# Performance work log

Hardware: AMD Instinct MI355X
Metric: run time of the kernel (lower is better)

The kernel has to match this reference:

```python
import jax, jax.numpy as jnp
import numpy as np
from jax.scipy.special import logsumexp

C = 1024   # num HMM states
H = 256    # hidden_dim
V = 10000  # vocab size
B = 16     # batch
N = 256    # sequence length
EPS = 1e-5


def _layernorm(x, g, b):
    mu = x.mean(-1, keepdims=True)
    var = ((x - mu) ** 2).mean(-1, keepdims=True)
    return g * (x - mu) * jax.lax.rsqrt(var + EPS) + b


def _residual(x, W1, b1, W2, b2, g, beta):
    # ResidualLayer: ln(relu(lin2(relu(lin1(x)))) + relu(lin1(x))), dropout=0
    h = jax.nn.relu(x @ W1.T + b1)
    return _layernorm(jax.nn.relu(h @ W2.T + b2) + h, g, beta)


def setup_inputs() -> dict:
    key = jax.random.key(0)
    ks = iter(jax.random.split(key, 40))
    def nrm(shape, scale):
        return jax.random.normal(next(ks), shape, dtype=jnp.float32) * scale
    w = 1.0 / np.sqrt(H)
    inp = {}
    # embeddings (torch.randn)
    inp['start_emb'] = nrm((C, H), 1.0)
    inp['state_emb'] = nrm((C, H), 1.0)
    inp['pre_emb'] = nrm((C, H), 1.0)
    # start_mlp: ResidualLayer(H,H) + Linear(H,1)
    for p, out_dim in (('s', 1), ('t', C), ('e', V)):
        inp[p + '_W1'] = nrm((H, H), w)
        inp[p + '_b1'] = jnp.zeros((H,), jnp.float32)
        inp[p + '_W2'] = nrm((H, H), w)
        inp[p + '_b2'] = jnp.zeros((H,), jnp.float32)
        inp[p + '_g'] = jnp.ones((H,), jnp.float32)
        inp[p + '_beta'] = jnp.zeros((H,), jnp.float32)
        inp[p + '_Wo'] = nrm((out_dim, H), w)
        inp[p + '_bo'] = jnp.zeros((out_dim,), jnp.float32)
    inp['text'] = jax.random.randint(next(ks), (B, N), 0, V)
    return inp


def reference(start_emb, state_emb, pre_emb,
              s_W1, s_b1, s_W2, s_b2, s_g, s_beta, s_Wo, s_bo,
              t_W1, t_b1, t_W2, t_b2, t_g, t_beta, t_Wo, t_bo,
              e_W1, e_b1, e_W2, e_b2, e_g, e_beta, e_Wo, e_bo,
              text):
    # start: (C,) log init distribution
    start = jax.nn.log_softmax(
        (_residual(start_emb, s_W1, s_b1, s_W2, s_b2, s_g, s_beta) @ s_Wo.T + s_bo).squeeze(-1))
    # transition[i, j] = log p(z_t = j | z_{t-1} = i), shape (C, C)
    transition = jax.nn.log_softmax(
        _residual(state_emb, t_W1, t_b1, t_W2, t_b2, t_g, t_beta) @ t_Wo.T + t_bo, axis=-1)
    # emission[c, v] = log p(x = v | z = c), shape (C, V)
    emission = jax.nn.log_softmax(
        _residual(pre_emb, e_W1, e_b1, e_W2, e_b2, e_g, e_beta) @ e_Wo.T + e_bo, axis=-1)

    emit = emission.T[text]              # (B, N, C): log p(x_t | z_t = c)
    alpha0 = start[None, :] + emit[:, 0]  # (B, C)

    def step(alpha, e_t):
        # log-semiring matmul: alpha_next[b,j] = lse_i(alpha[b,i] + T[i,j]) + emit
        a = logsumexp(alpha[:, :, None] + transition[None], axis=1) + e_t
        return a, None

    alphaT, _ = jax.lax.scan(step, alpha0, jnp.swapaxes(emit[:, 1:], 0, 1))
    return logsumexp(alphaT, axis=-1).sum()
```

## Files before the change

kernel.cpp:

```cpp
#include <hip/hip_runtime.h>
#include <hip/hip_bf16.h>

typedef __attribute__((ext_vector_type(8))) short short8;
typedef __attribute__((ext_vector_type(4))) float f32x4;
typedef unsigned short ushort;
typedef unsigned long long u64;
typedef unsigned int u32;

#define AL(p) __hip_atomic_load((p), __ATOMIC_RELAXED, __HIP_MEMORY_SCOPE_AGENT)
#define AS(p,v) __hip_atomic_store((p), (v), __ATOMIC_RELAXED, __HIP_MEMORY_SCOPE_AGENT)

__device__ inline ushort f2bf(float x) {
  __hip_bfloat16 h = __float2bfloat16(x);
  return *reinterpret_cast<ushort*>(&h);
}
__device__ inline float bfhi2f(u32 lo) {
  union { u32 u; float f; } c; c.u = lo & 0xFFFF0000u; return c.f;
}
__device__ inline float bflo2f(u32 lo) {
  union { u32 u; float f; } c; c.u = lo << 16; return c.f;
}
__device__ inline u32 pk2(float a, float b) {
  return (u32)f2bf(__expf(a)) | ((u32)f2bf(__expf(b)) << 16);
}

__global__ __launch_bounds__(256) void mlp3_kernel(
    const float* X0, const float* W10, const float* b10, const float* W20, const float* b20,
    const float* g0, const float* be0, float* of0, ushort* ob0,
    const float* X1, const float* W11, const float* b11, const float* W21, const float* b21,
    const float* g1, const float* be1, float* of1, ushort* ob1,
    const float* X2, const float* W12, const float* b12, const float* W22, const float* b22,
    const float* g2, const float* be2, float* of2, ushort* ob2,
    const float* ca_i, ushort* ca_o, int nc_a,
    const float* cb_i, ushort* cb_o, int nc_b)
{
  int y = blockIdx.y;
  if (y == 3) {
    int i = blockIdx.x * 256 + threadIdx.x;
    int st = 64 * 256;
    for (; i < nc_a + nc_b; i += st) {
      if (i < nc_a) ca_o[i] = f2bf(ca_i[i]);
      else          cb_o[i - nc_a] = f2bf(cb_i[i - nc_a]);
    }
    return;
  }
  const float *X, *W1, *b1, *W2, *b2, *g, *beta; float* of32; ushort* obf;
  if (y == 0)      { X=X0; W1=W10; b1=b10; W2=W20; b2=b20; g=g0; beta=be0; of32=of0; obf=ob0; }
  else if (y == 1) { X=X1; W1=W11; b1=b11; W2=W21; b2=b21; g=g1; beta=be1; of32=of1; obf=ob1; }
  else             { X=X2; W1=W12; b1=b12; W2=W22; b2=b22; g=g2; beta=be2; of32=of2; obf=ob2; }

  __shared__ float Xs[16 * 260];
  __shared__ float H1s[16 * 260];
  __shared__ float mu_s[16], rs_s[16];
  int tid = threadIdx.x;
  int r0 = blockIdx.x * 16;
  for (int q = 0; q < 16; ++q) Xs[q * 260 + tid] = X[(r0 + q) * 256 + tid];
  __syncthreads();
  int r = tid & 15, jg = tid >> 4;
  for (int jj = 0; jj < 16; ++jj) {
    int j = jg * 16 + jj;
    const float4* wrow = (const float4*)(W1 + j * 256);
    const float4* xrow = (const float4*)(Xs + r * 260);
    float acc = 0.f;
#pragma unroll 8
    for (int kq = 0; kq < 64; ++kq) {
      float4 w = wrow[kq], x = xrow[kq];
      acc += w.x * x.x + w.y * x.y + w.z * x.z + w.w * x.w;
    }
    acc += b1[j];
    H1s[r * 260 + j] = acc > 0.f ? acc : 0.f;
  }
  __syncthreads();
  for (int jj = 0; jj < 16; ++jj) {
    int j = jg * 16 + jj;
    const float4* wrow = (const float4*)(W2 + j * 256);
    const float4* hrow = (const float4*)(H1s + r * 260);
    float acc = 0.f;
#pragma unroll 8
    for (int kq = 0; kq < 64; ++kq) {
      float4 w = wrow[kq], x = hrow[kq];
      acc += w.x * x.x + w.y * x.y + w.z * x.z + w.w * x.w;
    }
    acc += b2[j];
    float v = (acc > 0.f ? acc : 0.f) + H1s[r * 260 + j];
    Xs[r * 260 + j] = v;
  }
  __syncthreads();
  if (tid < 16) {
    float s = 0.f, s2 = 0.f;
    for (int k = 0; k < 256; ++k) { float x = Xs[tid * 260 + k]; s += x; s2 += x * x; }
    float mu = s * (1.0f / 256.0f);
    float var = s2 * (1.0f / 256.0f) - mu * mu;
    mu_s[tid] = mu; rs_s[tid] = rsqrtf(var + 1e-5f);
  }
  __syncthreads();
  for (int q = 0; q < 16; ++q) {
    float x = (Xs[q * 260 + tid] - mu_s[q]) * rs_s[q] * g[tid] + beta[tid];
    if (of32) of32[(r0 + q) * 256 + tid] = x;
    if (obf)  obf[(r0 + q) * 256 + tid] = f2bf(x);
  }
}

__global__ __launch_bounds__(1024) void shead_kernel(
    const float* __restrict__ h, const float* __restrict__ Wo, const float* __restrict__ bo,
    float* __restrict__ start)
{
  __shared__ float red[16];
  __shared__ float lse_s;
  int tid = threadIdx.x;
  const float4* wr = (const float4*)Wo;
  const float4* hr = (const float4*)(h + tid * 256);
  float acc = 0.f;
  for (int kq = 0; kq < 64; ++kq) {
    float4 w = wr[kq], x = hr[kq];
    acc += w.x * x.x + w.y * x.y + w.z * x.z + w.w * x.w;
  }
  acc += bo[0];
  float s = __expf(acc);
  for (int m = 1; m < 64; m <<= 1) s += __shfl_xor(s, m);
  if ((tid & 63) == 0) red[tid >> 6] = s;
  __syncthreads();
  if (tid == 0) {
    float t = 0.f;
    for (int w = 0; w < 16; ++w) t += red[w];
    lse_s = logf(t);
  }
  __syncthreads();
  start[tid] = acc - lse_s;
}

__global__ __launch_bounds__(256) void gemm_kernel(
    const ushort* __restrict__ A, const ushort* __restrict__ Bw,
    int mode, int Nvalid, int chunks,
    const float* __restrict__ bias,
    float* __restrict__ out, float* __restrict__ esum, const int* __restrict__ text)
{
  __shared__ ushort As[64 * 264];
  __shared__ ushort Bs[32 * 264];
  int tid = threadIdx.x;
  int m0 = blockIdx.x * 64;
#pragma unroll
  for (int q = 0; q < 8; ++q) {
    int idx = q * 256 + tid;
    int row = idx >> 5, c8 = idx & 31;
    *(short8*)(As + row * 264 + c8 * 8) = *(const short8*)(A + (m0 + row) * 256 + c8 * 8);
  }
  int lane = tid & 63, wave = tid >> 6;
  int r16 = lane & 15, quad = lane >> 4;
  float sacc[4] = {0.f, 0.f, 0.f, 0.f};

  for (int c = 0; c < chunks; ++c) {
    int n0 = (blockIdx.y * chunks + c) * 32;
    if (c) __syncthreads();
#pragma unroll
    for (int q = 0; q < 4; ++q) {
      int idx = q * 256 + tid;
      int row = idx >> 5, c8 = idx & 31;
      int grow = n0 + row;
      short8 val = {0, 0, 0, 0, 0, 0, 0, 0};
      if (mode == 2) {
        int v = text[(grow & 15) * 256 + (grow >> 4)];
        val = *(const short8*)(Bw + v * 256 + c8 * 8);
      } else if (grow < Nvalid) {
        val = *(const short8*)(Bw + grow * 256 + c8 * 8);
      }
      *(short8*)(Bs + row * 264 + c8 * 8) = val;
    }
    __syncthreads();
    f32x4 acc0 = {0.f, 0.f, 0.f, 0.f}, acc1 = {0.f, 0.f, 0.f, 0.f};
#pragma unroll
    for (int kb = 0; kb < 8; ++kb) {
      short8 a  = *(const short8*)(As + (wave * 16 + r16) * 264 + kb * 32 + quad * 8);
      short8 b0 = *(const short8*)(Bs + r16 * 264 + kb * 32 + quad * 8);
      short8 b1 = *(const short8*)(Bs + (16 + r16) * 264 + kb * 32 + quad * 8);
      acc0 = __builtin_amdgcn_mfma_f32_16x16x32_bf16(a, b0, acc0, 0, 0, 0);
      acc1 = __builtin_amdgcn_mfma_f32_16x16x32_bf16(a, b1, acc1, 0, 0, 0);
    }
    if (mode == 0) {
#pragma unroll
      for (int rr = 0; rr < 4; ++rr) {
        int row = m0 + wave * 16 + quad * 4 + rr;
        int c0 = n0 + r16, c1 = n0 + 16 + r16;
        out[row * 1024 + c0] = acc0[rr] + bias[c0];
        out[row * 1024 + c1] = acc1[rr] + bias[c1];
      }
    } else if (mode == 1) {
#pragma unroll
      for (int rr = 0; rr < 4; ++rr) {
        int c0 = n0 + r16, c1 = n0 + 16 + r16;
        float p0 = (c0 < Nvalid) ? __expf(acc0[rr] + bias[c0]) : 0.f;
        float p1 = (c1 < Nvalid) ? __expf(acc1[rr] + bias[c1]) : 0.f;
        sacc[rr] += p0 + p1;
      }
    } else {
      int c0 = m0 + wave * 16 + quad * 4;
      int tb0 = n0 + r16, tb1 = n0 + 16 + r16;
      int v0 = text[(tb0 & 15) * 256 + (tb0 >> 4)];
      int v1 = text[(tb1 & 15) * 256 + (tb1 >> 4)];
      float l0 = logf(esum[c0]), l1 = logf(esum[c0 + 1]);
      float l2 = logf(esum[c0 + 2]), l3 = logf(esum[c0 + 3]);
      float4 o0, o1;
      o0.x = acc0[0] + bias[v0] - l0; o0.y = acc0[1] + bias[v0] - l1;
      o0.z = acc0[2] + bias[v0] - l2; o0.w = acc0[3] + bias[v0] - l3;
      o1.x = acc1[0] + bias[v1] - l0; o1.y = acc1[1] + bias[v1] - l1;
      o1.z = acc1[2] + bias[v1] - l2; o1.w = acc1[3] + bias[v1] - l3;
      *(float4*)(out + tb0 * 1024 + c0) = o0;
      *(float4*)(out + tb1 * 1024 + c0) = o1;
    }
  }
  if (mode == 1) {
#pragma unroll
    for (int rr = 0; rr < 4; ++rr) {
      float s = sacc[rr];
      s += __shfl_xor(s, 1); s += __shfl_xor(s, 2);
      s += __shfl_xor(s, 4); s += __shfl_xor(s, 8);
      if (r16 == 0) atomicAdd(esum + m0 + wave * 16 + quad * 4 + rr, s);
    }
  }
}

__global__ __launch_bounds__(256) void trans_kernel(
    const float* __restrict__ logits, ushort* __restrict__ texp_frag)
{
  __shared__ float red[4];
  __shared__ float lse_s;
  int i = blockIdx.x, tid = threadIdx.x;
  float x[4];
  float s = 0.f;
#pragma unroll
  for (int q = 0; q < 4; ++q) { x[q] = logits[i * 1024 + q * 256 + tid]; s += __expf(x[q]); }
  for (int m = 1; m < 64; m <<= 1) s += __shfl_xor(s, m);
  if ((tid & 63) == 0) red[tid >> 6] = s;
  __syncthreads();
  if (tid == 0) lse_s = logf(red[0] + red[1] + red[2] + red[3]);
  __syncthreads();
  float lse = lse_s;
  int kblk = i >> 5, quad = (i >> 3) & 3, idx = i & 7;
#pragma unroll
  for (int q = 0; q < 4; ++q) {
    int j = q * 256 + tid;
    int pos = (((j >> 4) * 32 + kblk) * 64 + quad * 16 + (j & 15)) * 8 + idx;
    texp_frag[pos] = f2bf(__expf(x[q] - lse));
  }
}

__global__ __launch_bounds__(256, 1) void scan_kernel(
    const ushort* __restrict__ texp_frag,
    const float* __restrict__ emitg,
    const float* __restrict__ start_v,
    u64* __restrict__ abuf,
    float* __restrict__ out)
{
  __shared__ __align__(16) char Asb[2][4 * 2080];
  __shared__ float redw[4][4], reds[4][4];

  int tid = threadIdx.x, lane = tid & 63, wave = tid >> 6;
  int r16 = lane & 15, quad = lane >> 4;
  int p = blockIdx.x, bg = p & 3, cb = p >> 2;
  int b0 = bg * 4;

  const short8* tg = (const short8*)texp_frag + (size_t)cb * 8192 + wave * 2048;
  short8 treg[32];
#pragma unroll
  for (int k = 0; k < 32; ++k) treg[k] = tg[k * 64 + lane];
#pragma unroll
  for (int k = 0; k < 32; ++k) asm volatile("" : "+a"(treg[k]));

  int colw = cb * 64 + wave * 16 + r16;
  int abase = (r16 & 3) * 2080 + quad * 16;

  float m_r[4], Bs[4];
#pragma unroll
  for (int i = 0; i < 4; ++i) {
    m_r[i] = start_v[0] + emitg[(size_t)(b0 + i) * 1024];
    Bs[i] = m_r[i];
  }
  {
    int c0 = 2 * tid, c2 = 2 * tid + 512;
    char* ab = Asb[1];
#pragma unroll
    for (int r = 0; r < 4; ++r) {
      const float* eb = emitg + (size_t)(b0 + r) * 1024;
      float v0 = start_v[c0] + eb[c0],     v1 = start_v[c0 + 1] + eb[c0 + 1];
      float v2 = start_v[c2] + eb[c2],     v3 = start_v[c2 + 1] + eb[c2 + 1];
      *(u32*)(ab + r * 2080 + 4 * tid)        = pk2(v0 - m_r[r], v1 - m_r[r]);
      *(u32*)(ab + r * 2080 + 1024 + 4 * tid) = pk2(v2 - m_r[r], v3 - m_r[r]);
    }
  }
  __syncthreads();

  for (int t = 1; t < 256; ++t) {
    float e0 = 0.f, e1 = 0.f, e2 = 0.f, e3 = 0.f;
    if (quad == 0) {
      const float* ep = emitg + (size_t)(t * 16 + b0) * 1024 + colw;
      e0 = ep[0]; e1 = ep[1024]; e2 = ep[2048]; e3 = ep[3072];
    }

    const char* ab = Asb[t & 1];
    f32x4 a0, a1, a2, a3;
    {
      short8 f0 = *(const short8*)(ab + abase);
      short8 f1 = *(const short8*)(ab + abase + 64);
      short8 f2 = *(const short8*)(ab + abase + 128);
      short8 f3 = *(const short8*)(ab + abase + 192);
      asm volatile("v_mfma_f32_16x16x32_bf16 %0, %1, %2, 0" : "=v"(a0) : "v"(f0), "a"(treg[0]));
      asm volatile("v_mfma_f32_16x16x32_bf16 %0, %1, %2, 0" : "=v"(a1) : "v"(f1), "a"(treg[1]));
      asm volatile("v_mfma_f32_16x16x32_bf16 %0, %1, %2, 0" : "=v"(a2) : "v"(f2), "a"(treg[2]));
      asm volatile("v_mfma_f32_16x16x32_bf16 %0, %1, %2, 0" : "=v"(a3) : "v"(f3), "a"(treg[3]));
    }
#pragma unroll
    for (int kb = 4; kb < 32; kb += 4) {
      short8 f0 = *(const short8*)(ab + abase + kb * 64);
      short8 f1 = *(const short8*)(ab + abase + kb * 64 + 64);
      short8 f2 = *(const short8*)(ab + abase + kb * 64 + 128);
      short8 f3 = *(const short8*)(ab + abase + kb * 64 + 192);
      asm volatile("v_mfma_f32_16x16x32_bf16 %0, %1, %2, %0" : "+v"(a0) : "v"(f0), "a"(treg[kb + 0]));
      asm volatile("v_mfma_f32_16x16x32_bf16 %0, %1, %2, %0" : "+v"(a1) : "v"(f1), "a"(treg[kb + 1]));
      asm volatile("v_mfma_f32_16x16x32_bf16 %0, %1, %2, %0" : "+v"(a2) : "v"(f2), "a"(treg[kb + 2]));
      asm volatile("v_mfma_f32_16x16x32_bf16 %0, %1, %2, %0" : "+v"(a3) : "v"(f3), "a"(treg[kb + 3]));
    }
    asm volatile("s_nop 7\n\ts_nop 7\n\ts_nop 1"
                 : "+v"(a0), "+v"(a1), "+v"(a2), "+v"(a3));
    f32x4 acc = (a0 + a1) + (a2 + a3);

    if (quad == 0) {
      float d0 = __logf(acc[0]) + e0;
      float d1 = __logf(acc[1]) + e1;
      float d2 = __logf(acc[2]) + e2;
      float d3 = __logf(acc[3]) + e3;
      u64 tag = ((u64)(u32)t) << 32;
      u64* ob = abuf + (t & 1) * 8192 + bg * 2048 + colw;
      AS(ob,        tag | (u64)((u32)f2bf(d0) | ((u32)f2bf(d1) << 16)));
      AS(ob + 1024, tag | (u64)((u32)f2bf(d2) | ((u32)f2bf(d3) << 16)));
    }

    if (t < 255) {
      u64 x0, x1, x2, x3, x4, x5, x6, x7, n0, n1;
      {
        const u64* buf = abuf + (t & 1) * 8192 + bg * 2048;
        int oa = 2 * tid, oc = 2 * tid + 512;
        u32 want = (u32)t;
        bool first = true;
        for (;;) {
          if (!first) __builtin_amdgcn_s_sleep(1);
          first = false;
          x0 = AL(buf + oa);        x1 = AL(buf + oa + 1);
          x2 = AL(buf + oc);        x3 = AL(buf + oc + 1);
          x4 = AL(buf + 1024 + oa); x5 = AL(buf + 1024 + oa + 1);
          x6 = AL(buf + 1024 + oc); x7 = AL(buf + 1024 + oc + 1);
          n0 = AL(buf);             n1 = AL(buf + 1024);
          u32 bad = ((u32)(x0 >> 32) ^ want) | ((u32)(x1 >> 32) ^ want) |
                    ((u32)(x2 >> 32) ^ want) | ((u32)(x3 >> 32) ^ want) |
                    ((u32)(x4 >> 32) ^ want) | ((u32)(x5 >> 32) ^ want) |
                    ((u32)(x6 >> 32) ^ want) | ((u32)(x7 >> 32) ^ want) |
                    ((u32)(n0 >> 32) ^ want) | ((u32)(n1 >> 32) ^ want);
          if (bad == 0) break;
        }
      }
      m_r[0] = bflo2f((u32)n0); m_r[1] = bfhi2f((u32)n0);
      m_r[2] = bflo2f((u32)n1); m_r[3] = bfhi2f((u32)n1);
      Bs[0] += m_r[0]; Bs[1] += m_r[1]; Bs[2] += m_r[2]; Bs[3] += m_r[3];

      char* aw = Asb[(t + 1) & 1];
      u32 l0 = (u32)x0, l1 = (u32)x1, l2 = (u32)x2, l3 = (u32)x3;
      u32 l4 = (u32)x4, l5 = (u32)x5, l6 = (u32)x6, l7 = (u32)x7;
      *(u32*)(aw + 4 * tid)                = pk2(bflo2f(l0) - m_r[0], bflo2f(l1) - m_r[0]);
      *(u32*)(aw + 1024 + 4 * tid)         = pk2(bflo2f(l2) - m_r[0], bflo2f(l3) - m_r[0]);
      *(u32*)(aw + 2080 + 4 * tid)         = pk2(bfhi2f(l0) - m_r[1], bfhi2f(l1) - m_r[1]);
      *(u32*)(aw + 2080 + 1024 + 4 * tid)  = pk2(bfhi2f(l2) - m_r[1], bfhi2f(l3) - m_r[1]);
      *(u32*)(aw + 4160 + 4 * tid)         = pk2(bflo2f(l4) - m_r[2], bflo2f(l5) - m_r[2]);
      *(u32*)(aw + 4160 + 1024 + 4 * tid)  = pk2(bflo2f(l6) - m_r[2], bflo2f(l7) - m_r[2]);
      *(u32*)(aw + 6240 + 4 * tid)         = pk2(bfhi2f(l4) - m_r[3], bfhi2f(l5) - m_r[3]);
      *(u32*)(aw + 6240 + 1024 + 4 * tid)  = pk2(bfhi2f(l6) - m_r[3], bfhi2f(l7) - m_r[3]);
      __syncthreads();
    }
  }

  if (cb == 0) {
    const u64* fb = abuf + 8192 + bg * 2048;
    int oa = 2 * tid, oc = 2 * tid + 512;
    u64 x0, x1, x2, x3, x4, x5, x6, x7;
    {
      bool first = true;
      for (;;) {
        if (!first) __builtin_amdgcn_s_sleep(1);
        first = false;
        x0 = AL(fb + oa);        x1 = AL(fb + oa + 1);
        x2 = AL(fb + oc);        x3 = AL(fb + oc + 1);
        x4 = AL(fb + 1024 + oa); x5 = AL(fb + 1024 + oa + 1);
        x6 = AL(fb + 1024 + oc); x7 = AL(fb + 1024 + oc + 1);
        u32 bad = ((u32)(x0 >> 32) ^ 255u) | ((u32)(x1 >> 32) ^ 255u) |
                  ((u32)(x2 >> 32) ^ 255u) | ((u32)(x3 >> 32) ^ 255u) |
                  ((u32)(x4 >> 32) ^ 255u) | ((u32)(x5 >> 32) ^ 255u) |
                  ((u32)(x6 >> 32) ^ 255u) | ((u32)(x7 >> 32) ^ 255u);
        if (bad == 0) break;
      }
    }
    float bv[4][4];
    bv[0][0] = bflo2f((u32)x0); bv[0][1] = bflo2f((u32)x1); bv[0][2] = bflo2f((u32)x2); bv[0][3] = bflo2f((u32)x3);
    bv[1][0] = bfhi2f((u32)x0); bv[1][1] = bfhi2f((u32)x1); bv[1][2] = bfhi2f((u32)x2); bv[1][3] = bfhi2f((u32)x3);
    bv[2][0] = bflo2f((u32)x4); bv[2][1] = bflo2f((u32)x5); bv[2][2] = bflo2f((u32)x6); bv[2][3] = bflo2f((u32)x7);
    bv[3][0] = bfhi2f((u32)x4); bv[3][1] = bfhi2f((u32)x5); bv[3][2] = bfhi2f((u32)x6); bv[3][3] = bfhi2f((u32)x7);
    float M[4], S[4];
#pragma unroll
    for (int i = 0; i < 4; ++i)
      M[i] = fmaxf(fmaxf(bv[i][0], bv[i][1]), fmaxf(bv[i][2], bv[i][3]));
    for (int off = 1; off < 64; off <<= 1) {
#pragma unroll
      for (int i = 0; i < 4; ++i) M[i] = fmaxf(M[i], __shfl_xor(M[i], off));
    }
    if (lane == 0) { redw[wave][0]=M[0]; redw[wave][1]=M[1]; redw[wave][2]=M[2]; redw[wave][3]=M[3]; }
    __syncthreads();
#pragma unroll
    for (int i = 0; i < 4; ++i)
      M[i] = fmaxf(fmaxf(redw[0][i], redw[1][i]), fmaxf(redw[2][i], redw[3][i]));
#pragma unroll
    for (int i = 0; i < 4; ++i)
      S[i] = __expf(bv[i][0] - M[i]) + __expf(bv[i][1] - M[i]) +
             __expf(bv[i][2] - M[i]) + __expf(bv[i][3] - M[i]);
    for (int off = 1; off < 64; off <<= 1) {
#pragma unroll
      for (int i = 0; i < 4; ++i) S[i] += __shfl_xor(S[i], off);
    }
    if (lane == 0) { reds[wave][0]=S[0]; reds[wave][1]=S[1]; reds[wave][2]=S[2]; reds[wave][3]=S[3]; }
    __syncthreads();
    if (tid == 0) {
      float tot = 0.f;
#pragma unroll
      for (int i = 0; i < 4; ++i) {
        float Sg = reds[0][i] + reds[1][i] + reds[2][i] + reds[3][i];
        tot += Bs[i] + M[i] + logf(Sg);
      }
      atomicAdd(out, tot);
    }
  }
}

extern "C" void kernel_launch(void* const* d_in, const int* in_sizes, int n_in,
                              void* d_out, int out_size, void* d_ws, size_t ws_size,
                              hipStream_t stream)
{
  (void)in_sizes; (void)n_in; (void)out_size; (void)ws_size;
  const float* start_emb = (const float*)d_in[0];
  const float* state_emb = (const float*)d_in[1];
  const float* pre_emb   = (const float*)d_in[2];
  const float* s_W1 = (const float*)d_in[3];  const float* s_b1 = (const float*)d_in[4];
  const float* s_W2 = (const float*)d_in[5];  const float* s_b2 = (const float*)d_in[6];
  const float* s_g  = (const float*)d_in[7];  const float* s_be = (const float*)d_in[8];
  const float* s_Wo = (const float*)d_in[9];  const float* s_bo = (const float*)d_in[10];
  const float* t_W1 = (const float*)d_in[11]; const float* t_b1 = (const float*)d_in[12];
  const float* t_W2 = (const float*)d_in[13]; const float* t_b2 = (const float*)d_in[14];
  const float* t_g  = (const float*)d_in[15]; const float* t_be = (const float*)d_in[16];
  const float* t_Wo = (const float*)d_in[17]; const float* t_bo = (const float*)d_in[18];
  const float* e_W1 = (const float*)d_in[19]; const float* e_b1 = (const float*)d_in[20];
  const float* e_W2 = (const float*)d_in[21]; const float* e_b2 = (const float*)d_in[22];
  const float* e_g  = (const float*)d_in[23]; const float* e_be = (const float*)d_in[24];
  const float* e_Wo = (const float*)d_in[25]; const float* e_bo = (const float*)d_in[26];
  const int*   text = (const int*)d_in[27];
  float* out = (float*)d_out;

  char* ws = (char*)d_ws;
  size_t off = 0;
  auto alloc = [&](size_t bytes) -> char* {
    char* p = ws + off;
    off = (off + bytes + 255) & ~(size_t)255;
    return p;
  };
  float* esum       = (float*)alloc(1024 * 4);
  u64*   abuf       = (u64*)alloc(2 * 8192 * 8);
  float* start_v    = (float*)alloc(1024 * 4);
  float* h_s        = (float*)alloc(1024 * 256 * 4);
  ushort* h_t_bf    = (ushort*)alloc(1024 * 256 * 2);
  ushort* h_e_bf    = (ushort*)alloc(1024 * 256 * 2);
  ushort* tWo_bf    = (ushort*)alloc(1024 * 256 * 2);
  ushort* eWo_bf    = (ushort*)alloc(10000 * 256 * 2);
  float* tlogits    = (float*)alloc(1024 * 1024 * 4);
  ushort* texp_frag = (ushort*)alloc(1024 * 1024 * 2);
  float* emitg      = (float*)alloc(4096 * 1024 * 4);

  hipMemsetAsync(ws, 0, 4096 + 2 * 8192 * 8, stream);
  hipMemsetAsync(d_out, 0, 4, stream);

  mlp3_kernel<<<dim3(64, 4), 256, 0, stream>>>(
      start_emb, s_W1, s_b1, s_W2, s_b2, s_g, s_be, h_s, nullptr,
      state_emb, t_W1, t_b1, t_W2, t_b2, t_g, t_be, nullptr, h_t_bf,
      pre_emb,  e_W1, e_b1, e_W2, e_b2, e_g, e_be, nullptr, h_e_bf,
      t_Wo, tWo_bf, 1024 * 256, e_Wo, eWo_bf, 10000 * 256);

  shead_kernel<<<1, 1024, 0, stream>>>(h_s, s_Wo, s_bo, start_v);

  gemm_kernel<<<dim3(16, 32),  256, 0, stream>>>(h_t_bf, tWo_bf, 0, 1024,  1, t_bo, tlogits, nullptr, nullptr);
  trans_kernel<<<1024, 256, 0, stream>>>(tlogits, texp_frag);
  gemm_kernel<<<dim3(16, 40),  256, 0, stream>>>(h_e_bf, eWo_bf, 1, 10000, 8, e_bo, nullptr, esum, nullptr);
  gemm_kernel<<<dim3(16, 128), 256, 0, stream>>>(h_e_bf, eWo_bf, 2, 4096,  1, e_bo, emitg, esum, text);

  scan_kernel<<<64, 256, 0, stream>>>(texp_frag, emitg, start_v, abuf, out);
}
```

Before: 913.8 us.

## Halve scan blocks; each wave computes two 16-column transition tiles

```diff
diff --git a/kernel.cpp b/kernel.cpp
--- a/kernel.cpp
+++ b/kernel.cpp
@@ -259,14 +259,18 @@
   int p = blockIdx.x, bg = p & 3, cb = p >> 2;
   int b0 = bg * 4;
 
-  const short8* tg = (const short8*)texp_frag + (size_t)cb * 8192 + wave * 2048;
-  short8 treg[32];
-#pragma unroll
-  for (int k = 0; k < 32; ++k) treg[k] = tg[k * 64 + lane];
-#pragma unroll
-  for (int k = 0; k < 32; ++k) asm volatile("" : "+a"(treg[k]));
-
-  int colw = cb * 64 + wave * 16 + r16;
+  const short8* tg = (const short8*)texp_frag + (size_t)(cb * 8 + wave * 2) * 2048;
+  short8 tA[32], tB[32];
+#pragma unroll
+  for (int k = 0; k < 32; ++k) tA[k] = tg[k * 64 + lane];
+#pragma unroll
+  for (int k = 0; k < 32; ++k) tB[k] = tg[2048 + k * 64 + lane];
+#pragma unroll
+  for (int k = 0; k < 32; ++k) asm volatile("" : "+a"(tA[k]));
+#pragma unroll
+  for (int k = 0; k < 32; ++k) asm volatile("" : "+a"(tB[k]));
+
+  int colw = cb * 128 + wave * 32 + r16;
   int abase = (r16 & 3) * 2080 + quad * 16;
 
   float m_r[4], Bs[4];
@@ -291,22 +295,28 @@
 
   for (int t = 1; t < 256; ++t) {
     float e0 = 0.f, e1 = 0.f, e2 = 0.f, e3 = 0.f;
+    float e4 = 0.f, e5 = 0.f, e6 = 0.f, e7 = 0.f;
     if (quad == 0) {
       const float* ep = emitg + (size_t)(t * 16 + b0) * 1024 + colw;
-      e0 = ep[0]; e1 = ep[1024]; e2 = ep[2048]; e3 = ep[3072];
+      e0 = ep[0];  e1 = ep[1024]; e2 = ep[2048]; e3 = ep[3072];
+      e4 = ep[16]; e5 = ep[1040]; e6 = ep[2064]; e7 = ep[3088];
     }
 
     const char* ab = Asb[t & 1];
-    f32x4 a0, a1, a2, a3;
+    f32x4 a0, a1, a2, a3, c0, c1, c2, c3;
     {
       short8 f0 = *(const short8*)(ab + abase);
       short8 f1 = *(const short8*)(ab + abase + 64);
       short8 f2 = *(const short8*)(ab + abase + 128);
       short8 f3 = *(const short8*)(ab + abase + 192);
-      asm volatile("v_mfma_f32_16x16x32_bf16 %0, %1, %2, 0" : "=v"(a0) : "v"(f0), "a"(treg[0]));
-      asm volatile("v_mfma_f32_16x16x32_bf16 %0, %1, %2, 0" : "=v"(a1) : "v"(f1), "a"(treg[1]));
-      asm volatile("v_mfma_f32_16x16x32_bf16 %0, %1, %2, 0" : "=v"(a2) : "v"(f2), "a"(treg[2]));
-      asm volatile("v_mfma_f32_16x16x32_bf16 %0, %1, %2, 0" : "=v"(a3) : "v"(f3), "a"(treg[3]));
+      asm volatile("v_mfma_f32_16x16x32_bf16 %0, %1, %2, 0" : "=v"(a0) : "v"(f0), "a"(tA[0]));
+      asm volatile("v_mfma_f32_16x16x32_bf16 %0, %1, %2, 0" : "=v"(a1) : "v"(f1), "a"(tA[1]));
+      asm volatile("v_mfma_f32_16x16x32_bf16 %0, %1, %2, 0" : "=v"(a2) : "v"(f2), "a"(tA[2]));
+      asm volatile("v_mfma_f32_16x16x32_bf16 %0, %1, %2, 0" : "=v"(a3) : "v"(f3), "a"(tA[3]));
+      asm volatile("v_mfma_f32_16x16x32_bf16 %0, %1, %2, 0" : "=v"(c0) : "v"(f0), "a"(tB[0]));
+      asm volatile("v_mfma_f32_16x16x32_bf16 %0, %1, %2, 0" : "=v"(c1) : "v"(f1), "a"(tB[1]));
+      asm volatile("v_mfma_f32_16x16x32_bf16 %0, %1, %2, 0" : "=v"(c2) : "v"(f2), "a"(tB[2]));
+      asm volatile("v_mfma_f32_16x16x32_bf16 %0, %1, %2, 0" : "=v"(c3) : "v"(f3), "a"(tB[3]));
     }
 #pragma unroll
     for (int kb = 4; kb < 32; kb += 4) {
@@ -314,24 +324,36 @@
       short8 f1 = *(const short8*)(ab + abase + kb * 64 + 64);
       short8 f2 = *(const short8*)(ab + abase + kb * 64 + 128);
       short8 f3 = *(const short8*)(ab + abase + kb * 64 + 192);
-      asm volatile("v_mfma_f32_16x16x32_bf16 %0, %1, %2, %0" : "+v"(a0) : "v"(f0), "a"(treg[kb + 0]));
-      asm volatile("v_mfma_f32_16x16x32_bf16 %0, %1, %2, %0" : "+v"(a1) : "v"(f1), "a"(treg[kb + 1]));
-      asm volatile("v_mfma_f32_16x16x32_bf16 %0, %1, %2, %0" : "+v"(a2) : "v"(f2), "a"(treg[kb + 2]));
-      asm volatile("v_mfma_f32_16x16x32_bf16 %0, %1, %2, %0" : "+v"(a3) : "v"(f3), "a"(treg[kb + 3]));
+      asm volatile("v_mfma_f32_16x16x32_bf16 %0, %1, %2, %0" : "+v"(a0) : "v"(f0), "a"(tA[kb + 0]));
+      asm volatile("v_mfma_f32_16x16x32_bf16 %0, %1, %2, %0" : "+v"(a1) : "v"(f1), "a"(tA[kb + 1]));
+      asm volatile("v_mfma_f32_16x16x32_bf16 %0, %1, %2, %0" : "+v"(a2) : "v"(f2), "a"(tA[kb + 2]));
+      asm volatile("v_mfma_f32_16x16x32_bf16 %0, %1, %2, %0" : "+v"(a3) : "v"(f3), "a"(tA[kb + 3]));
+      asm volatile("v_mfma_f32_16x16x32_bf16 %0, %1, %2, %0" : "+v"(c0) : "v"(f0), "a"(tB[kb + 0]));
+      asm volatile("v_mfma_f32_16x16x32_bf16 %0, %1, %2, %0" : "+v"(c1) : "v"(f1), "a"(tB[kb + 1]));
+      asm volatile("v_mfma_f32_16x16x32_bf16 %0, %1, %2, %0" : "+v"(c2) : "v"(f2), "a"(tB[kb + 2]));
+      asm volatile("v_mfma_f32_16x16x32_bf16 %0, %1, %2, %0" : "+v"(c3) : "v"(f3), "a"(tB[kb + 3]));
     }
     asm volatile("s_nop 7\n\ts_nop 7\n\ts_nop 1"
-                 : "+v"(a0), "+v"(a1), "+v"(a2), "+v"(a3));
-    f32x4 acc = (a0 + a1) + (a2 + a3);
+                 : "+v"(a0), "+v"(a1), "+v"(a2), "+v"(a3),
+                   "+v"(c0), "+v"(c1), "+v"(c2), "+v"(c3));
+    f32x4 accA = (a0 + a1) + (a2 + a3);
+    f32x4 accB = (c0 + c1) + (c2 + c3);
 
     if (quad == 0) {
-      float d0 = __logf(acc[0]) + e0;
-      float d1 = __logf(acc[1]) + e1;
-      float d2 = __logf(acc[2]) + e2;
-      float d3 = __logf(acc[3]) + e3;
+      float d0 = __logf(accA[0]) + e0;
+      float d1 = __logf(accA[1]) + e1;
+      float d2 = __logf(accA[2]) + e2;
+      float d3 = __logf(accA[3]) + e3;
+      float d4 = __logf(accB[0]) + e4;
+      float d5 = __logf(accB[1]) + e5;
+      float d6 = __logf(accB[2]) + e6;
+      float d7 = __logf(accB[3]) + e7;
       u64 tag = ((u64)(u32)t) << 32;
       u64* ob = abuf + (t & 1) * 8192 + bg * 2048 + colw;
-      AS(ob,        tag | (u64)((u32)f2bf(d0) | ((u32)f2bf(d1) << 16)));
-      AS(ob + 1024, tag | (u64)((u32)f2bf(d2) | ((u32)f2bf(d3) << 16)));
+      AS(ob,             tag | (u64)((u32)f2bf(d0) | ((u32)f2bf(d1) << 16)));
+      AS(ob + 1024,      tag | (u64)((u32)f2bf(d2) | ((u32)f2bf(d3) << 16)));
+      AS(ob + 16,        tag | (u64)((u32)f2bf(d4) | ((u32)f2bf(d5) << 16)));
+      AS(ob + 16 + 1024, tag | (u64)((u32)f2bf(d6) | ((u32)f2bf(d7) << 16)));
     }
 
     if (t < 255) {
@@ -494,5 +516,5 @@
   gemm_kernel<<<dim3(16, 40),  256, 0, stream>>>(h_e_bf, eWo_bf, 1, 10000, 8, e_bo, nullptr, esum, nullptr);
   gemm_kernel<<<dim3(16, 128), 256, 0, stream>>>(h_e_bf, eWo_bf, 2, 4096,  1, e_bo, emitg, esum, text);
 
-  scan_kernel<<<64, 256, 0, stream>>>(texp_frag, emitg, start_v, abuf, out);
-}
+  scan_kernel<<<32, 256, 0, stream>>>(texp_frag, emitg, start_v, abuf, out);
+}
```

New measurement: 927.3 us. No clear change (+1.5%).
